# Optimization experiments

Hardware: AMD Instinct MI355X
Metric: run time of the kernel (lower is better)

The kernel has to match this reference:

```python
import jax, jax.numpy as jnp
import numpy as np

B, S, D, H = 2, 2048, 1024, 16
HD = D // H
SCALE_FACTOR = 0.2  # ScalableSoftmax scale


def setup_inputs() -> dict:
    key = jax.random.key(0)
    ks = jax.random.split(key, 5)
    inv = 1.0 / np.sqrt(D)
    return {
        "x": jax.random.normal(ks[0], (B, S, D), dtype=jnp.float32),
        "qkv_w": jax.random.normal(ks[1], (3 * D, D), dtype=jnp.float32) * inv,
        "qkv_b": jax.random.normal(ks[2], (3 * D,), dtype=jnp.float32) * 0.02,
        "out_w": jax.random.normal(ks[3], (D, D), dtype=jnp.float32) * inv,
        "out_b": jax.random.normal(ks[4], (D,), dtype=jnp.float32) * 0.02,
    }


def reference(x, qkv_w, qkv_b, out_w, out_b):
    b, s, d = x.shape
    # qkv projection: [b, s, 3d] -> [b, h, s, 3*hd]
    qkv = (jnp.einsum("bsd,ed->bse", x, qkv_w) + qkv_b)
    qkv = qkv.reshape(b, s, H, 3 * HD).transpose(0, 2, 1, 3)
    q, k, v = jnp.split(qkv, 3, axis=-1)  # each [b, h, s, hd]
    # scaled dot-product scores, then ScalableSoftmax: softmax(0.2 * scores)
    scores = jnp.einsum("bhqd,bhkd->bhqk", q, k) / jnp.sqrt(jnp.float32(HD))
    attn = jax.nn.softmax(SCALE_FACTOR * scores, axis=-1)
    vals = jnp.einsum("bhqk,bhkd->bhqd", attn, v)
    vals = vals.transpose(0, 2, 1, 3).reshape(b, s, d)
    return jnp.einsum("bsd,ed->bse", vals, out_w) + out_b
```

## Files before the change

### kernel.cpp

```cpp
#include <hip/hip_runtime.h>

using bh8    = __attribute__((ext_vector_type(8)))  short;
using f32x4v = __attribute__((ext_vector_type(4)))  float;
using f32x16 = __attribute__((ext_vector_type(16))) float;
using u32x4  = __attribute__((ext_vector_type(4)))  unsigned int;
using us4    = __attribute__((ext_vector_type(4)))  unsigned short;

#define AS1 __attribute__((address_space(1)))
#define AS3 __attribute__((address_space(3)))

#define B_  2
#define S_  2048
#define D_  1024
#define H_  16
#define HD_ 64
#define C2A 0.0360673760222241f

__device__ __forceinline__ unsigned short f2bf(float f) {
  unsigned u = __builtin_bit_cast(unsigned, f);
  return (unsigned short)((u + 0x7fffu + ((u >> 16) & 1u)) >> 16);
}
__device__ __forceinline__ int swz8(int r) { return (r ^ (r >> 3)) & 7; }

__global__ __launch_bounds__(256) void cvt_all(const float* __restrict__ x,
                                               const float* __restrict__ qw,
                                               const float* __restrict__ ow,
                                               unsigned short* __restrict__ xb,
                                               unsigned short* __restrict__ qwb,
                                               unsigned short* __restrict__ owb) {
  int i = blockIdx.x * 256 + threadIdx.x;
  const float* src; unsigned short* dst; int off;
  if (i < 1048576)      { src = x;  dst = xb;  off = i; }
  else if (i < 1835008) { src = qw; dst = qwb; off = i - 1048576; }
  else                  { src = ow; dst = owb; off = i - 1835008; }
  f32x4v v = reinterpret_cast<const f32x4v*>(src)[off];
  us4 o;
  o[0] = f2bf(v[0]); o[1] = f2bf(v[1]); o[2] = f2bf(v[2]); o[3] = f2bf(v[3]);
  reinterpret_cast<us4*>(dst)[off] = o;
}

template <int MODE, int BM, int GX, int NW>
__global__ __launch_bounds__(256) void gemm_bt(const unsigned short* __restrict__ A,
                                               const unsigned short* __restrict__ Bw,
                                               const float* __restrict__ bias,
                                               float* __restrict__ Cf,
                                               unsigned short* __restrict__ Qo,
                                               unsigned short* __restrict__ Ko,
                                               unsigned short* __restrict__ Vo,
                                               int M, int N, int K) {
  constexpr int NIW = (BM == 128) ? 4 : 2;
  constexpr int NA  = BM / 32;
  __shared__ __align__(16) short As[BM * 64];
  __shared__ __align__(16) short Bs[128 * 64];
  const int tid = threadIdx.x;
  const int w = tid >> 6, l = tid & 63;
  const int lr = l & 15, lg = l >> 4;
  const int lin = blockIdx.y * GX + blockIdx.x;
  const int sw  = (lin & 7) * (NW / 8) + (lin >> 3);
  const int m0 = (sw % GX) * BM, n0 = (sw / GX) * 128;
  const int wm = (BM == 128) ? (w >> 1) * 64 : 0;
  const int wn = (BM == 128) ? (w & 1) * 64 : w * 32;

  f32x4v acc[4][NIW];
#pragma unroll
  for (int a = 0; a < 4; a++)
#pragma unroll
    for (int b = 0; b < NIW; b++)
#pragma unroll
      for (int r = 0; r < 4; r++) acc[a][b][r] = 0.f;

#pragma unroll 1
  for (int k0 = 0; k0 < K; k0 += 64) {
    __syncthreads();
#pragma unroll
    for (int n = 0; n < NA; n++) {
      int idx = n * 256 + tid;
      int row = idx >> 3, p = idx & 7;
      int c = p ^ swz8(row);
      const unsigned short* srcA = A + (size_t)(m0 + row) * K + k0 + c * 8;
      __builtin_amdgcn_global_load_lds((const AS1 void*)srcA,
          (AS3 void*)((char*)As + (n * 256 + w * 64) * 16), 16, 0, 0);
    }
#pragma unroll
    for (int n = 0; n < 4; n++) {
      int idx = n * 256 + tid;
      int row = idx >> 3, p = idx & 7;
      int c = p ^ swz8(row);
      const unsigned short* srcB = Bw + (size_t)(n0 + row) * K + k0 + c * 8;
      __builtin_amdgcn_global_load_lds((const AS1 void*)srcB,
          (AS3 void*)((char*)Bs + (n * 256 + w * 64) * 16), 16, 0, 0);
    }
    __syncthreads();
#pragma unroll
    for (int kk = 0; kk < 2; kk++) {
      bh8 af[4], bf[NIW];
#pragma unroll
      for (int mi = 0; mi < 4; mi++) {
        int row = wm + mi * 16 + lr;
        int slot = (4 * kk + lg) ^ swz8(row);
        af[mi] = *(const bh8*)((const char*)As + row * 128 + slot * 16);
      }
#pragma unroll
      for (int ni = 0; ni < NIW; ni++) {
        int row = wn + ni * 16 + lr;
        int slot = (4 * kk + lg) ^ swz8(row);
        bf[ni] = *(const bh8*)((const char*)Bs + row * 128 + slot * 16);
      }
#pragma unroll
      for (int mi = 0; mi < 4; mi++)
#pragma unroll
        for (int ni = 0; ni < NIW; ni++)
          acc[mi][ni] = __builtin_amdgcn_mfma_f32_16x16x32_bf16(af[mi], bf[ni], acc[mi][ni], 0, 0, 0);
    }
  }

  if (MODE == 1) {
#pragma unroll
    for (int ni = 0; ni < NIW; ni++) {
      int e = n0 + wn + ni * 16 + lr;
      float bv = bias[e];
#pragma unroll
      for (int mi = 0; mi < 4; mi++) {
        int mbase = m0 + wm + mi * 16 + lg * 4;
#pragma unroll
        for (int r = 0; r < 4; r++)
          Cf[(size_t)(mbase + r) * N + e] = acc[mi][ni][r] + bv;
      }
    }
  } else {
#pragma unroll
    for (int ni = 0; ni < NIW; ni++) {
      int e = n0 + wn + ni * 16 + lr;
      int hh = e / 192;
      int rr = e - hh * 192;
      int tsel = rr >> 6, d = rr & 63;
      float bv = bias[e];
#pragma unroll
      for (int mi = 0; mi < 4; mi++) {
        int mbase = m0 + wm + mi * 16 + lg * 4;
#pragma unroll
        for (int r = 0; r < 4; r++) {
          int m = mbase + r;
          int b = m >> 11, s = m & 2047;
          float val = acc[mi][ni][r] + bv;
          size_t bh = (size_t)(b * H_ + hh);
          if (tsel == 0)      Qo[(bh * S_ + s) * HD_ + d] = f2bf(val * C2A);
          else if (tsel == 1) Ko[(bh * S_ + s) * HD_ + d] = f2bf(val);
          else                Vo[(bh * HD_ + d) * S_ + s] = f2bf(val);
        }
      }
    }
  }
}

__global__ __launch_bounds__(512) void attn_fwd(const unsigned short* __restrict__ Qt,
                                                const unsigned short* __restrict__ Kt,
                                                const unsigned short* __restrict__ VT,
                                                unsigned short* __restrict__ vals) {
  __shared__ __align__(16) short Ks[2 * 2 * 64 * 64];
  __shared__ __align__(16) short Vs[2 * 2 * 64 * 64];
  const int tid = threadIdx.x, w = tid >> 6, l = tid & 63;
  const int lq = l & 31, h = l >> 5;
  const int lin = blockIdx.x;
  const int uu_ = lin >> 3;
  const int bh = (lin & 7) + 8 * (uu_ & 3);
  const int q0 = (uu_ >> 2) * 256 + w * 32;
  const unsigned short* Qp = Qt + (size_t)bh * (S_ * HD_);
  const unsigned short* Kp = Kt + (size_t)bh * (S_ * HD_);
  const unsigned short* Vp = VT + (size_t)bh * (HD_ * S_);

  bh8 qf[4];
#pragma unroll
  for (int kf = 0; kf < 4; kf++)
    qf[kf] = *(const bh8*)(Qp + (size_t)(q0 + lq) * HD_ + kf * 16 + h * 8);

  f32x16 KZ;
#pragma unroll
  for (int r = 0; r < 16; r++) KZ[r] = 0.f;
  bh8 ones;
#pragma unroll
  for (int j = 0; j < 8; j++) ones[j] = (short)0x3F80;

  f32x16 O[2], Ol;
  O[0] = KZ; O[1] = KZ; Ol = KZ;

  const int row0 = tid >> 3, cc = (tid & 7) ^ swz8(row0);
  const unsigned short* kp0 = Kp + row0 * HD_ + cc * 8;
  const unsigned short* vp0 = Vp + (size_t)row0 * S_ + cc * 8;
  char* dK = (char*)Ks + w * 1024;
  char* dV = (char*)Vs + w * 1024;

  auto stage = [&](int i, int buf) {
    const unsigned short* kB = kp0 + (size_t)i * 8192;
    const unsigned short* vB = vp0 + (size_t)i * 128;
    __builtin_amdgcn_global_load_lds((const AS1 void*)kB,
                                     (AS3 void*)(dK + buf * 16384), 16, 0, 0);
    __builtin_amdgcn_global_load_lds((const AS1 void*)(kB + 4096),
                                     (AS3 void*)(dK + buf * 16384 + 8192), 16, 0, 0);
    __builtin_amdgcn_global_load_lds((const AS1 void*)vB,
                                     (AS3 void*)(dV + buf * 16384), 16, 0, 0);
    __builtin_amdgcn_global_load_lds((const AS1 void*)(vB + 64),
                                     (AS3 void*)(dV + buf * 16384 + 8192), 16, 0, 0);
  };

  int ko0[4], ko1[4], vo0[4], vo1[4];
#pragma unroll
  for (int kf = 0; kf < 4; kf++) {
    int r0 = lq, r1 = 32 + lq;
    ko0[kf] = r0 * 128 + (((2 * kf + h) ^ swz8(r0)) << 4);
    ko1[kf] = r1 * 128 + (((2 * kf + h) ^ swz8(r1)) << 4);
  }
#pragma unroll
  for (int c = 0; c < 2; c++)
#pragma unroll
    for (int ni = 0; ni < 2; ni++) {
      int d = ni * 32 + lq;
      vo0[c * 2 + ni] = d * 128 + (((2 * c + h) ^ swz8(d)) << 4);
      vo1[c * 2 + ni] = d * 128 + (((4 + 2 * c + h) ^ swz8(d)) << 4);
    }

  stage(0, 0);
#pragma unroll 1
  for (int i = 0; i < 16; i++) {
    const int cur = i & 1;
    asm volatile("s_waitcnt vmcnt(0)" ::: "memory");
    __builtin_amdgcn_s_barrier();
    if (i < 15) stage(i + 1, cur ^ 1);
#pragma unroll
    for (int tt = 0; tt < 2; tt++) {
      const char* Kc = (const char*)Ks + cur * 16384 + tt * 8192;
      const char* Vc = (const char*)Vs + cur * 16384 + tt * 8192;

      f32x16 sa, sb;
      __builtin_amdgcn_s_setprio(1);
      {
        bh8 k0 = *(const bh8*)(Kc + ko0[0]);
        bh8 k1 = *(const bh8*)(Kc + ko1[0]);
        sa = __builtin_amdgcn_mfma_f32_32x32x16_bf16(k0, qf[0], KZ, 0, 0, 0);
        sb = __builtin_amdgcn_mfma_f32_32x32x16_bf16(k1, qf[0], KZ, 0, 0, 0);
      }
#pragma unroll
      for (int kf = 1; kf < 4; kf++) {
        bh8 k0 = *(const bh8*)(Kc + ko0[kf]);
        bh8 k1 = *(const bh8*)(Kc + ko1[kf]);
        sa = __builtin_amdgcn_mfma_f32_32x32x16_bf16(k0, qf[kf], sa, 0, 0, 0);
        sb = __builtin_amdgcn_mfma_f32_32x32x16_bf16(k1, qf[kf], sb, 0, 0, 0);
      }
      __builtin_amdgcn_s_setprio(0);

      float pa_[16], pb_[16];
#pragma unroll
      for (int r = 0; r < 16; r++)
        asm("v_exp_f32 %0, %1" : "=v"(pa_[r]) : "v"(sa[r]));
      unsigned wa0[4], wa1[4];
#pragma unroll
      for (int g = 0; g < 4; g++) {
        asm("v_cvt_pk_bf16_f32 %0, %1, %2" : "=v"(wa0[g]) : "v"(pa_[4 * g]), "v"(pa_[4 * g + 1]));
        asm("v_cvt_pk_bf16_f32 %0, %1, %2" : "=v"(wa1[g]) : "v"(pa_[4 * g + 2]), "v"(pa_[4 * g + 3]));
      }
#pragma unroll
      for (int r = 0; r < 16; r++)
        asm("v_exp_f32 %0, %1" : "=v"(pb_[r]) : "v"(sb[r]));
      unsigned wb0[4], wb1[4];
#pragma unroll
      for (int g = 0; g < 4; g++) {
        asm("v_cvt_pk_bf16_f32 %0, %1, %2" : "=v"(wb0[g]) : "v"(pb_[4 * g]), "v"(pb_[4 * g + 1]));
        asm("v_cvt_pk_bf16_f32 %0, %1, %2" : "=v"(wb1[g]) : "v"(pb_[4 * g + 2]), "v"(pb_[4 * g + 3]));
      }

      bh8 paf[2], pbf[2];
#pragma unroll
      for (int c = 0; c < 2; c++) {
        unsigned x0 = wa0[2 * c], y0 = wa0[2 * c + 1];
        unsigned x1 = wa1[2 * c], y1 = wa1[2 * c + 1];
        asm("v_permlane32_swap_b32 %0, %1" : "+v"(x0), "+v"(y0));
        asm("v_permlane32_swap_b32 %0, %1" : "+v"(x1), "+v"(y1));
        u32x4 up; up[0] = x0; up[1] = x1; up[2] = y0; up[3] = y1;
        paf[c] = __builtin_bit_cast(bh8, up);
      }
#pragma unroll
      for (int c = 0; c < 2; c++) {
        unsigned x0 = wb0[2 * c], y0 = wb0[2 * c + 1];
        unsigned x1 = wb1[2 * c], y1 = wb1[2 * c + 1];
        asm("v_permlane32_swap_b32 %0, %1" : "+v"(x0), "+v"(y0));
        asm("v_permlane32_swap_b32 %0, %1" : "+v"(x1), "+v"(y1));
        u32x4 up; up[0] = x0; up[1] = x1; up[2] = y0; up[3] = y1;
        pbf[c] = __builtin_bit_cast(bh8, up);
      }

      __builtin_amdgcn_s_setprio(1);
#pragma unroll
      for (int c = 0; c < 2; c++) {
        bh8 vf0 = *(const bh8*)(Vc + vo0[c * 2 + 0]);
        bh8 vf1 = *(const bh8*)(Vc + vo0[c * 2 + 1]);
        O[0] = __builtin_amdgcn_mfma_f32_32x32x16_bf16(paf[c], vf0, O[0], 0, 0, 0);
        O[1] = __builtin_amdgcn_mfma_f32_32x32x16_bf16(paf[c], vf1, O[1], 0, 0, 0);
        Ol   = __builtin_amdgcn_mfma_f32_32x32x16_bf16(paf[c], ones, Ol, 0, 0, 0);
      }
#pragma unroll
      for (int c = 0; c < 2; c++) {
        bh8 vf0 = *(const bh8*)(Vc + vo1[c * 2 + 0]);
        bh8 vf1 = *(const bh8*)(Vc + vo1[c * 2 + 1]);
        O[0] = __builtin_amdgcn_mfma_f32_32x32x16_bf16(pbf[c], vf0, O[0], 0, 0, 0);
        O[1] = __builtin_amdgcn_mfma_f32_32x32x16_bf16(pbf[c], vf1, O[1], 0, 0, 0);
        Ol   = __builtin_amdgcn_mfma_f32_32x32x16_bf16(pbf[c], ones, Ol, 0, 0, 0);
      }
      __builtin_amdgcn_s_setprio(0);
    }
  }

  float rl[16];
#pragma unroll
  for (int r = 0; r < 16; r++) rl[r] = __builtin_amdgcn_rcpf(Ol[r]);

  const int b = bh >> 4, hh = bh & 15;
#pragma unroll
  for (int ni = 0; ni < 2; ni++) {
    int d = ni * 32 + lq;
#pragma unroll
    for (int r = 0; r < 16; r++) {
      float vvv = O[ni][r] * rl[r];
      int qg = q0 + 4 * h + 8 * (r >> 2) + (r & 3);
      vals[((size_t)(b * S_ + qg)) * D_ + hh * HD_ + d] = f2bf(vvv);
    }
  }
}

extern "C" void kernel_launch(void* const* d_in, const int* in_sizes, int n_in,
                              void* d_out, int out_size, void* d_ws, size_t ws_size,
                              hipStream_t stream) {
  const float* x     = (const float*)d_in[0];
  const float* qkv_w = (const float*)d_in[1];
  const float* qkv_b = (const float*)d_in[2];
  const float* out_w = (const float*)d_in[3];
  const float* out_b = (const float*)d_in[4];
  float* out = (float*)d_out;

  unsigned short* xb  = (unsigned short*)d_ws;
  unsigned short* qwb = xb  + (size_t)4096 * 1024;
  unsigned short* owb = qwb + (size_t)3072 * 1024;
  unsigned short* Qb  = owb + (size_t)1024 * 1024;
  unsigned short* Kb  = Qb  + (size_t)32 * 2048 * 64;
  unsigned short* Vb  = Kb  + (size_t)32 * 2048 * 64;
  unsigned short* vb  = Vb  + (size_t)32 * 2048 * 64;

  cvt_all<<<8192, 256, 0, stream>>>(x, qkv_w, out_w, xb, qwb, owb);
  gemm_bt<0, 128, 32, 768><<<dim3(32, 24), 256, 0, stream>>>(xb, qwb, qkv_b, nullptr, Qb, Kb, Vb,
                                                             4096, 3072, 1024);
  attn_fwd<<<256, 512, 0, stream>>>(Qb, Kb, Vb, vb);
  gemm_bt<1, 64, 64, 512><<<dim3(64, 8), 256, 0, stream>>>(vb, owb, out_b, out, nullptr, nullptr, nullptr,
                                                           4096, 1024, 1024);
}
```

Measured before the change: 107.2 us.

## Split attention over two key halves and add a combine kernel

The attention kernel now splits each query tile's key range into two halves, doubling the grid from 256 to 512 blocks, so the 256 CUs of the device get more work per CU. Each half writes unnormalized bf16 partial outputs and row sums, reusing the xb and qwb workspace buffers. A new combine kernel adds the partials and divides by the total row sum. The conversion kernel also processes four elements per thread with fewer blocks. This costs an extra round trip of the partials through memory, one more launch, and an extra bf16 rounding of the unnormalized partials. Because softmax skips the max subtraction, the halves can be summed directly without any rescaling.

```diff
diff --git a/kernel.cpp b/kernel.cpp
--- a/kernel.cpp
+++ b/kernel.cpp
@@ -20,6 +20,9 @@
   unsigned u = __builtin_bit_cast(unsigned, f);
   return (unsigned short)((u + 0x7fffu + ((u >> 16) & 1u)) >> 16);
 }
+__device__ __forceinline__ float bf2f(unsigned short v) {
+  return __builtin_bit_cast(float, (unsigned)v << 16);
+}
 __device__ __forceinline__ int swz8(int r) { return (r ^ (r >> 3)) & 7; }
 
 __global__ __launch_bounds__(256) void cvt_all(const float* __restrict__ x,
@@ -28,15 +31,18 @@
                                                unsigned short* __restrict__ xb,
                                                unsigned short* __restrict__ qwb,
                                                unsigned short* __restrict__ owb) {
-  int i = blockIdx.x * 256 + threadIdx.x;
-  const float* src; unsigned short* dst; int off;
-  if (i < 1048576)      { src = x;  dst = xb;  off = i; }
-  else if (i < 1835008) { src = qw; dst = qwb; off = i - 1048576; }
-  else                  { src = ow; dst = owb; off = i - 1835008; }
-  f32x4v v = reinterpret_cast<const f32x4v*>(src)[off];
-  us4 o;
-  o[0] = f2bf(v[0]); o[1] = f2bf(v[1]); o[2] = f2bf(v[2]); o[3] = f2bf(v[3]);
-  reinterpret_cast<us4*>(dst)[off] = o;
+#pragma unroll
+  for (int it = 0; it < 4; it++) {
+    int i = it * 524288 + blockIdx.x * 256 + threadIdx.x;
+    const float* src; unsigned short* dst; int off;
+    if (i < 1048576)      { src = x;  dst = xb;  off = i; }
+    else if (i < 1835008) { src = qw; dst = qwb; off = i - 1048576; }
+    else                  { src = ow; dst = owb; off = i - 1835008; }
+    f32x4v v = reinterpret_cast<const f32x4v*>(src)[off];
+    us4 o;
+    o[0] = f2bf(v[0]); o[1] = f2bf(v[1]); o[2] = f2bf(v[2]); o[3] = f2bf(v[3]);
+    reinterpret_cast<us4*>(dst)[off] = o;
+  }
 }
 
 template <int MODE, int BM, int GX, int NW>
@@ -156,7 +162,9 @@
 __global__ __launch_bounds__(512) void attn_fwd(const unsigned short* __restrict__ Qt,
                                                 const unsigned short* __restrict__ Kt,
                                                 const unsigned short* __restrict__ VT,
-                                                unsigned short* __restrict__ vals) {
+                                                unsigned short* __restrict__ P0,
+                                                unsigned short* __restrict__ P1,
+                                                float* __restrict__ Lp) {
   __shared__ __align__(16) short Ks[2 * 2 * 64 * 64];
   __shared__ __align__(16) short Vs[2 * 2 * 64 * 64];
   const int tid = threadIdx.x, w = tid >> 6, l = tid & 63;
@@ -164,7 +172,10 @@
   const int lin = blockIdx.x;
   const int uu_ = lin >> 3;
   const int bh = (lin & 7) + 8 * (uu_ & 3);
-  const int q0 = (uu_ >> 2) * 256 + w * 32;
+  const int rest = uu_ >> 2;
+  const int q0 = (rest >> 1) * 256 + w * 32;
+  const int part = rest & 1;
+  const int tbase = part * 1024;
   const unsigned short* Qp = Qt + (size_t)bh * (S_ * HD_);
   const unsigned short* Kp = Kt + (size_t)bh * (S_ * HD_);
   const unsigned short* Vp = VT + (size_t)bh * (HD_ * S_);
@@ -185,8 +196,8 @@
   O[0] = KZ; O[1] = KZ; Ol = KZ;
 
   const int row0 = tid >> 3, cc = (tid & 7) ^ swz8(row0);
-  const unsigned short* kp0 = Kp + row0 * HD_ + cc * 8;
-  const unsigned short* vp0 = Vp + (size_t)row0 * S_ + cc * 8;
+  const unsigned short* kp0 = Kp + (size_t)(tbase + row0) * HD_ + cc * 8;
+  const unsigned short* vp0 = Vp + (size_t)row0 * S_ + tbase + cc * 8;
   char* dK = (char*)Ks + w * 1024;
   char* dV = (char*)Vs + w * 1024;
 
@@ -221,11 +232,11 @@
 
   stage(0, 0);
 #pragma unroll 1
-  for (int i = 0; i < 16; i++) {
+  for (int i = 0; i < 8; i++) {
     const int cur = i & 1;
     asm volatile("s_waitcnt vmcnt(0)" ::: "memory");
     __builtin_amdgcn_s_barrier();
-    if (i < 15) stage(i + 1, cur ^ 1);
+    if (i < 7) stage(i + 1, cur ^ 1);
 #pragma unroll
     for (int tt = 0; tt < 2; tt++) {
       const char* Kc = (const char*)Ks + cur * 16384 + tt * 8192;
@@ -309,21 +320,44 @@
     }
   }
 
-  float rl[16];
-#pragma unroll
-  for (int r = 0; r < 16; r++) rl[r] = __builtin_amdgcn_rcpf(Ol[r]);
-
+  unsigned short* po = part ? P1 : P0;
   const int b = bh >> 4, hh = bh & 15;
 #pragma unroll
   for (int ni = 0; ni < 2; ni++) {
     int d = ni * 32 + lq;
 #pragma unroll
     for (int r = 0; r < 16; r++) {
-      float vvv = O[ni][r] * rl[r];
       int qg = q0 + 4 * h + 8 * (r >> 2) + (r & 3);
-      vals[((size_t)(b * S_ + qg)) * D_ + hh * HD_ + d] = f2bf(vvv);
-    }
-  }
+      po[((size_t)(b * S_ + qg)) * D_ + hh * HD_ + d] = f2bf(O[ni][r]);
+    }
+  }
+  if (lq == 0) {
+#pragma unroll
+    for (int r = 0; r < 16; r++) {
+      int qg = q0 + 4 * h + 8 * (r >> 2) + (r & 3);
+      Lp[part * 65536 + bh * 2048 + qg] = Ol[r];
+    }
+  }
+}
+
+__global__ __launch_bounds__(256) void combine(const unsigned short* __restrict__ P1,
+                                               const float* __restrict__ Lp,
+                                               unsigned short* __restrict__ P0out) {
+  int i = blockIdx.x * 256 + threadIdx.x;
+  int e4 = i << 2;
+  int hhd = e4 & 1023;
+  int s   = (e4 >> 10) & 2047;
+  int b   = e4 >> 21;
+  int hh  = hhd >> 6;
+  int li  = (b * H_ + hh) * S_ + s;
+  float rl = __builtin_amdgcn_rcpf(Lp[li] + Lp[65536 + li]);
+  us4 a = reinterpret_cast<const us4*>(P0out)[i];
+  us4 c = reinterpret_cast<const us4*>(P1)[i];
+  us4 o;
+#pragma unroll
+  for (int j = 0; j < 4; j++)
+    o[j] = f2bf((bf2f(a[j]) + bf2f(c[j])) * rl);
+  reinterpret_cast<us4*>(P0out)[i] = o;
 }
 
 extern "C" void kernel_launch(void* const* d_in, const int* in_sizes, int n_in,
@@ -344,10 +378,11 @@
   unsigned short* Vb  = Kb  + (size_t)32 * 2048 * 64;
   unsigned short* vb  = Vb  + (size_t)32 * 2048 * 64;
 
-  cvt_all<<<8192, 256, 0, stream>>>(x, qkv_w, out_w, xb, qwb, owb);
+  cvt_all<<<2048, 256, 0, stream>>>(x, qkv_w, out_w, xb, qwb, owb);
   gemm_bt<0, 128, 32, 768><<<dim3(32, 24), 256, 0, stream>>>(xb, qwb, qkv_b, nullptr, Qb, Kb, Vb,
                                                              4096, 3072, 1024);
-  attn_fwd<<<256, 512, 0, stream>>>(Qb, Kb, Vb, vb);
+  attn_fwd<<<512, 512, 0, stream>>>(Qb, Kb, Vb, vb, xb, (float*)qwb);
+  combine<<<4096, 256, 0, stream>>>(xb, (float*)qwb, vb);
   gemm_bt<1, 64, 64, 512><<<dim3(64, 8), 256, 0, stream>>>(vb, owb, out_b, out, nullptr, nullptr, nullptr,
                                                            4096, 1024, 1024);
 }
```

After: 115.2 us. 1.07x slower.
